# Optimization experiments

Hardware: AMD Instinct MI355X
Metric: run time of the kernel (lower is better)

## Reference

```python
import jax, jax.numpy as jnp
import numpy as np

EMBED = 1024
HEADS = 16
HEAD_DIM = EMBED // HEADS
BATCH = 4
SEQ = 2048


def setup_inputs() -> dict:
    key = jax.random.key(0)
    ks = jax.random.split(key, 9)
    s = 1.0 / np.sqrt(EMBED)
    inp = {
        "x": jax.random.normal(ks[0], (BATCH, SEQ, EMBED), dtype=jnp.float32),
        "Wq": jax.random.normal(ks[1], (EMBED, EMBED), dtype=jnp.float32) * s,
        "bq": jnp.zeros((EMBED,), jnp.float32),
        "Wk": jax.random.normal(ks[2], (EMBED, EMBED), dtype=jnp.float32) * s,
        "bk": jnp.zeros((EMBED,), jnp.float32),
        "Wv": jax.random.normal(ks[3], (EMBED, EMBED), dtype=jnp.float32) * s,
        "bv": jnp.zeros((EMBED,), jnp.float32),
        "Wo": jax.random.normal(ks[4], (EMBED, EMBED), dtype=jnp.float32) * s,
        "bo": jnp.zeros((EMBED,), jnp.float32),
    }
    return inp


def reference(x, Wq, bq, Wk, bk, Wv, bv, Wo, bo):
    B, S, E = x.shape
    H, D = HEADS, HEAD_DIM
    # projections (torch Linear with weight stored as [in,out] here)
    q = (x @ Wq + bq).reshape(B, S, H, D).transpose(0, 2, 1, 3)  # [B,H,S,D]
    k = (x @ Wk + bk).reshape(B, S, H, D).transpose(0, 2, 1, 3)
    v = (x @ Wv + bv).reshape(B, S, H, D).transpose(0, 2, 1, 3)
    scores = jnp.einsum('bhqd,bhkd->bhqk', q, k) * (1.0 / np.sqrt(D))
    causal = jnp.tril(jnp.ones((S, S), dtype=bool))
    scores = jnp.where(causal[None, None], scores, -jnp.inf)
    attn = jax.nn.softmax(scores, axis=-1)  # dropout p=0.0 -> identity
    out = jnp.einsum('bhqk,bhkd->bhqd', attn, v)  # [B,H,S,D]
    out = out.transpose(0, 2, 1, 3).reshape(B, S, E)
    return out @ Wo + bo
```

## Files before the change

### kernel.cpp

```cpp
#include <hip/hip_runtime.h>
#include <stdint.h>

#define EMBED 1024
#define SEQ   2048
#define BATCH 4
#define HEADS 16
#define HDIM  64
#define LDP   72

typedef unsigned short ushort_t;
typedef __bf16 bf16x8 __attribute__((ext_vector_type(8)));
typedef __bf16 bf16x4 __attribute__((ext_vector_type(4)));
typedef float  f32x4  __attribute__((ext_vector_type(4)));
typedef float  f32x16 __attribute__((ext_vector_type(16)));

#define MFMA16 __builtin_amdgcn_mfma_f32_16x16x32_bf16
#define MFMA32 __builtin_amdgcn_mfma_f32_32x32x16_bf16

typedef __attribute__((address_space(3))) uint32_t lds_u32_t;
typedef __attribute__((address_space(1))) const uint32_t glb_u32_t;

__device__ __forceinline__ void gl_lds16(const ushort_t* g, ushort_t* l) {
    __builtin_amdgcn_global_load_lds((glb_u32_t*)g, (lds_u32_t*)l, 16, 0, 0);
}

__device__ __forceinline__ ushort_t f2bf(float f) {
    union { float f; uint32_t u; } c; c.f = f;
    uint32_t u = c.u;
    return (ushort_t)((u + 0x7FFFu + ((u >> 16) & 1u)) >> 16);
}

__device__ __forceinline__ float exp2f_fast(float x) {
    float r; asm("v_exp_f32 %0, %1" : "=v"(r) : "v"(x)); return r;
}

__global__ __launch_bounds__(256)
void cast_x(const float* __restrict__ X, ushort_t* __restrict__ Xb)
{
    size_t i = ((size_t)blockIdx.x * 256 + threadIdx.x) * 8;
    ushort_t tmp[8];
    #pragma unroll
    for (int e = 0; e < 8; ++e) tmp[e] = f2bf(X[i + e]);
    *(uint4*)(Xb + i) = *(const uint4*)tmp;
}

__global__ __launch_bounds__(256)
void cast_transpose_w(const float* __restrict__ W, ushort_t* __restrict__ Wt)
{
    __shared__ ushort_t Ts[64 * 80];
    const int t = threadIdx.x;
    const int k0 = blockIdx.x * 64, n0 = blockIdx.y * 64;
    const int r = t >> 2, cs = (t & 3) * 16;
    const float* src = W + (size_t)(k0 + r) * EMBED + n0 + cs;
    #pragma unroll
    for (int e = 0; e < 16; ++e) Ts[(cs + e) * 80 + r] = f2bf(src[e]);
    __syncthreads();
    const int n = t >> 2, ks = (t & 3) * 16;
    ushort_t* dst = Wt + (size_t)(n0 + n) * EMBED + k0 + ks;
    *(uint4*)(dst)     = *(const uint4*)(&Ts[n * 80 + ks]);
    *(uint4*)(dst + 8) = *(const uint4*)(&Ts[n * 80 + ks + 8]);
}

__global__ __launch_bounds__(256)
void gemm_qkv(const ushort_t* __restrict__ A, const ushort_t* __restrict__ Bt,
              const float* __restrict__ bq, const float* __restrict__ bk,
              const float* __restrict__ bv, ushort_t* __restrict__ Cq, size_t tsz)
{
    __shared__ ushort_t As[128 * 32];
    __shared__ ushort_t Bs[128 * 32];
    const int t = threadIdx.x;
    const int wave = t >> 6, lane = t & 63;
    const int l15 = lane & 15, quad = lane >> 4;
    const int m0 = blockIdx.y * 128, n0 = blockIdx.x * 128;
    const int wm = (wave >> 1) * 64, wn = (wave & 1) * 64;
    f32x4 acc[4][4] = {};

    const int srow = wave * 32 + (lane >> 2), scol = (lane & 3) * 8;
    const ushort_t* Ag = A  + (size_t)(m0 + srow) * EMBED + scol;
    const ushort_t* Bg = Bt + (size_t)(n0 + srow) * EMBED + scol;
    ushort_t* AsW = As + wave * 1024;
    ushort_t* BsW = Bs + wave * 1024;

    for (int k0 = 0; k0 < EMBED; k0 += 32) {
        gl_lds16(Ag + k0,              AsW);
        gl_lds16(Ag + k0 + 16 * EMBED, AsW + 512);
        gl_lds16(Bg + k0,              BsW);
        gl_lds16(Bg + k0 + 16 * EMBED, BsW + 512);
        __syncthreads();

        bf16x8 af[4], bfr[4];
        #pragma unroll
        for (int mt = 0; mt < 4; ++mt)
            af[mt] = *(const bf16x8*)(&As[(wm + mt * 16 + l15) * 32 + quad * 8]);
        #pragma unroll
        for (int nt = 0; nt < 4; ++nt)
            bfr[nt] = *(const bf16x8*)(&Bs[(wn + nt * 16 + l15) * 32 + quad * 8]);
        #pragma unroll
        for (int mt = 0; mt < 4; ++mt)
            #pragma unroll
            for (int nt = 0; nt < 4; ++nt)
                acc[mt][nt] = MFMA16(af[mt], bfr[nt], acc[mt][nt], 0, 0, 0);
        __syncthreads();
    }

    const int mat = blockIdx.x >> 3;
    const float* bias = (mat == 0) ? bq : (mat == 1) ? bk : bv;
    const float scale = (mat == 0) ? 0.18033688011112042f : 1.0f;
    ushort_t* C = Cq + (size_t)mat * tsz;
    const int nc0 = (blockIdx.x & 7) * 128;
    #pragma unroll
    for (int nt = 0; nt < 4; ++nt) {
        int col = nc0 + wn + nt * 16 + l15;
        float bb = bias[col];
        #pragma unroll
        for (int mt = 0; mt < 4; ++mt)
            #pragma unroll
            for (int r = 0; r < 4; ++r) {
                int row = m0 + wm + mt * 16 + quad * 4 + r;
                C[(size_t)row * EMBED + col] = f2bf((acc[mt][nt][r] + bb) * scale);
            }
    }
}

__global__ __launch_bounds__(256)
void gemm_o(const ushort_t* __restrict__ A, const ushort_t* __restrict__ Bt,
            const float* __restrict__ bias, float* __restrict__ C)
{
    __shared__ ushort_t As[128 * 32];
    __shared__ ushort_t Bs[128 * 32];
    const int t = threadIdx.x;
    const int wave = t >> 6, lane = t & 63;
    const int l15 = lane & 15, quad = lane >> 4;
    const int m0 = blockIdx.y * 128, n0 = blockIdx.x * 128;
    const int wm = (wave >> 1) * 64, wn = (wave & 1) * 64;
    f32x4 acc[4][4] = {};

    const int srow = wave * 32 + (lane >> 2), scol = (lane & 3) * 8;
    const ushort_t* Ag = A  + (size_t)(m0 + srow) * EMBED + scol;
    const ushort_t* Bg = Bt + (size_t)(n0 + srow) * EMBED + scol;
    ushort_t* AsW = As + wave * 1024;
    ushort_t* BsW = Bs + wave * 1024;

    for (int k0 = 0; k0 < EMBED; k0 += 32) {
        gl_lds16(Ag + k0,              AsW);
        gl_lds16(Ag + k0 + 16 * EMBED, AsW + 512);
        gl_lds16(Bg + k0,              BsW);
        gl_lds16(Bg + k0 + 16 * EMBED, BsW + 512);
        __syncthreads();

        bf16x8 af[4], bfr[4];
        #pragma unroll
        for (int mt = 0; mt < 4; ++mt)
            af[mt] = *(const bf16x8*)(&As[(wm + mt * 16 + l15) * 32 + quad * 8]);
        #pragma unroll
        for (int nt = 0; nt < 4; ++nt)
            bfr[nt] = *(const bf16x8*)(&Bs[(wn + nt * 16 + l15) * 32 + quad * 8]);
        #pragma unroll
        for (int mt = 0; mt < 4; ++mt)
            #pragma unroll
            for (int nt = 0; nt < 4; ++nt)
                acc[mt][nt] = MFMA16(af[mt], bfr[nt], acc[mt][nt], 0, 0, 0);
        __syncthreads();
    }

    #pragma unroll
    for (int nt = 0; nt < 4; ++nt) {
        int col = n0 + wn + nt * 16 + l15;
        float bb = bias[col];
        #pragma unroll
        for (int mt = 0; mt < 4; ++mt)
            #pragma unroll
            for (int r = 0; r < 4; ++r) {
                int row = m0 + wm + mt * 16 + quad * 4 + r;
                C[(size_t)row * EMBED + col] = acc[mt][nt][r] + bb;
            }
    }
}

__global__ __launch_bounds__(256)
void transpose_v(const ushort_t* __restrict__ V, ushort_t* __restrict__ Vt)
{
    int blk = blockIdx.x;
    int st = blk & 31, bh = blk >> 5;
    int h = bh & 15, b = bh >> 4;
    int s0 = st * 64;
    __shared__ ushort_t Ts[64 * LDP];
    int tid = threadIdx.x;
    int r = tid >> 2, g = (tid & 3) * 8;

    const ushort_t* src = V + ((size_t)(b * SEQ + s0 + r)) * EMBED + h * HDIM;
    uint4 v0 = *(const uint4*)(src + g);
    uint4 v1 = *(const uint4*)(src + g + 32);
    const ushort_t* e0 = (const ushort_t*)&v0;
    const ushort_t* e1 = (const ushort_t*)&v1;
    #pragma unroll
    for (int e = 0; e < 8; ++e) Ts[(g + e) * LDP + r] = e0[e];
    #pragma unroll
    for (int e = 0; e < 8; ++e) Ts[(g + 32 + e) * LDP + r] = e1[e];
    __syncthreads();

    int d = tid >> 2;
    ushort_t* dst = Vt + ((size_t)bh * HDIM + d) * SEQ + s0;
    *(uint4*)(dst + g)      = *(const uint4*)(&Ts[d * LDP + g]);
    *(uint4*)(dst + g + 32) = *(const uint4*)(&Ts[d * LDP + g + 32]);
}

__global__ __launch_bounds__(512, 4)
void flash_attn(const ushort_t* __restrict__ Q, const ushort_t* __restrict__ K,
                const ushort_t* __restrict__ Vt, ushort_t* __restrict__ O)
{
    const int xcd = blockIdx.x & 7, c = blockIdx.x >> 3;
    const int p  = 15 - (c >> 3);
    const int bh = xcd * 8 + (c & 7);
    const int h = bh & 15, b = bh >> 4;
    const int t = threadIdx.x, w = t >> 6, lane = t & 63;
    const int wl = w & 3, hf = w >> 2;
    const int l31 = lane & 31, hi = lane >> 5;
    const int s = 4 * p + wl;
    const int sdiag = s >> 1;
    const int odd = s & 1;
    const int R = p + 1;
    const int jt0 = hf ? (p + 1) : 0;
    const size_t qkbase = (size_t)b * SEQ * EMBED + (size_t)h * HDIM;
    const size_t vtbase = (size_t)bh * HDIM * SEQ;

    __shared__ __attribute__((aligned(16))) ushort_t smem[32768];

    bf16x8 qb[4];
    {
        const ushort_t* qrow = Q + qkbase + (size_t)(s * 32 + l31) * EMBED + hi * 8;
        #pragma unroll
        for (int ks = 0; ks < 4; ++ks) qb[ks] = *(const bf16x8*)(qrow + ks * 16);
    }

    union { uint32_t u[4]; bf16x8 v; } onesu;
    onesu.u[0] = onesu.u[1] = onesu.u[2] = onesu.u[3] = 0x3F803F80u;
    const bf16x8 ones = onesu.v;

    const int rr = lane >> 3, cc = lane & 7;
    const ushort_t* Kg = K  + qkbase + (size_t)(jt0 * 64 + wl * 16 + rr) * EMBED + ((cc ^ rr) * 8);
    const ushort_t* Vg = Vt + vtbase + (size_t)(wl * 16 + rr) * SEQ + jt0 * 64 + ((cc ^ rr) * 8);

    f32x16 o0 = {}, o1 = {}, lac = {};
    const int swz = l31 & 7;

    {
        ushort_t* kd = smem + (hf * 2 + 0) * 4096 + wl * 1024;
        ushort_t* vd = smem + 16384 + (hf * 2 + 0) * 4096 + wl * 1024;
        gl_lds16(Kg,             kd);
        gl_lds16(Kg + 8 * EMBED, kd + 512);
        gl_lds16(Vg,             vd);
        gl_lds16(Vg + 8 * SEQ,   vd + 512);
    }

    for (int r = 0; r < R; ++r) {
        const int cur = r & 1;
        __syncthreads();

        if (r + 1 < R) {
            const ushort_t* kg = Kg + (size_t)(r + 1) * 64 * EMBED;
            const ushort_t* vg = Vg + (r + 1) * 64;
            ushort_t* kd = smem + (hf * 2 + (cur ^ 1)) * 4096 + wl * 1024;
            ushort_t* vd = smem + 16384 + (hf * 2 + (cur ^ 1)) * 4096 + wl * 1024;
            gl_lds16(kg,             kd);
            gl_lds16(kg + 8 * EMBED, kd + 512);
            gl_lds16(vg,             vd);
            gl_lds16(vg + 8 * SEQ,   vd + 512);
        }

        const int jt = jt0 + r;
        if (jt <= sdiag) {
            const ushort_t* Kst = smem + (hf * 2 + cur) * 4096;
            const ushort_t* Vst = smem + 16384 + (hf * 2 + cur) * 4096;
            const bool dg = (jt == sdiag);
            const bool skip1 = dg && !odd;

            f32x16 st0 = {}, st1 = {};
            #pragma unroll
            for (int ks = 0; ks < 4; ++ks) {
                bf16x8 k0 = *(const bf16x8*)(Kst + l31 * 64 + (((ks * 2 + hi) ^ swz) * 8));
                st0 = MFMA32(k0, qb[ks], st0, 0, 0, 0);
            }
            if (!skip1) {
                #pragma unroll
                for (int ks = 0; ks < 4; ++ks) {
                    bf16x8 k1 = *(const bf16x8*)(Kst + (32 + l31) * 64 + (((ks * 2 + hi) ^ swz) * 8));
                    st1 = MFMA32(k1, qb[ks], st1, 0, 0, 0);
                }
            }

            bf16x8 pa0 = {}, pa1 = {}, pa2 = {}, pa3 = {};
            {
                float p0[16];
                #pragma unroll
                for (int r2 = 0; r2 < 16; ++r2) p0[r2] = exp2f_fast(st0[r2]);
                if (dg && !odd) {
                    #pragma unroll
                    for (int r2 = 0; r2 < 16; ++r2) {
                        int key = (r2 & 3) + 8 * (r2 >> 2) + 4 * hi;
                        if (key > l31) p0[r2] = 0.f;
                    }
                }
                #pragma unroll
                for (int e = 0; e < 8; ++e) { pa0[e] = (__bf16)p0[e]; pa1[e] = (__bf16)p0[8 + e]; }
                if (!skip1) {
                    float p1[16];
                    #pragma unroll
                    for (int r2 = 0; r2 < 16; ++r2) p1[r2] = exp2f_fast(st1[r2]);
                    if (dg && odd) {
                        #pragma unroll
                        for (int r2 = 0; r2 < 16; ++r2) {
                            int key = (r2 & 3) + 8 * (r2 >> 2) + 4 * hi;
                            if (key > l31) p1[r2] = 0.f;
                        }
                    }
                    #pragma unroll
                    for (int e = 0; e < 8; ++e) { pa2[e] = (__bf16)p1[e]; pa3[e] = (__bf16)p1[8 + e]; }
                }
            }

            #pragma unroll
            for (int ksl = 0; ksl < 4; ++ksl) {
                if (!(ksl >= 2 && skip1)) {
                    bf16x8 pf = (ksl == 0) ? pa0 : (ksl == 1) ? pa1 : (ksl == 2) ? pa2 : pa3;
                    const int c0 = (((ksl * 2)     ^ swz) * 8) + hi * 4;
                    const int c1 = (((ksl * 2 + 1) ^ swz) * 8) + hi * 4;
                    union { bf16x4 hh[2]; bf16x8 v; } u0, u1;
                    u0.hh[0] = *(const bf16x4*)(Vst + l31 * 64 + c0);
                    u0.hh[1] = *(const bf16x4*)(Vst + l31 * 64 + c1);
                    u1.hh[0] = *(const bf16x4*)(Vst + (32 + l31) * 64 + c0);
                    u1.hh[1] = *(const bf16x4*)(Vst + (32 + l31) * 64 + c1);
                    o0  = MFMA32(pf, u0.v, o0, 0, 0, 0);
                    o1  = MFMA32(pf, u1.v, o1, 0, 0, 0);
                    lac = MFMA32(pf, ones, lac, 0, 0, 0);
                }
            }
        }
    }

    __syncthreads();
    float* Cs = (float*)smem;
    if (hf) {
        float* dst = Cs + (wl * 64 + lane) * 49;
        #pragma unroll
        for (int r2 = 0; r2 < 16; ++r2) {
            dst[r2]      = o0[r2];
            dst[16 + r2] = o1[r2];
            dst[32 + r2] = lac[r2];
        }
    }
    __syncthreads();
    if (!hf) {
        const float* src = Cs + (wl * 64 + lane) * 49;
        #pragma unroll
        for (int r2 = 0; r2 < 16; ++r2) {
            float t0 = o0[r2]  + src[r2];
            float t1 = o1[r2]  + src[16 + r2];
            float lt = lac[r2] + src[32 + r2];
            float inv = 1.0f / lt;
            int q = (r2 & 3) + 8 * (r2 >> 2) + 4 * hi;
            size_t ob = qkbase + (size_t)(s * 32 + q) * EMBED;
            O[ob + l31]      = f2bf(t0 * inv);
            O[ob + 32 + l31] = f2bf(t1 * inv);
        }
    }
}

extern "C" void kernel_launch(void* const* d_in, const int* in_sizes, int n_in,
                              void* d_out, int out_size, void* d_ws, size_t ws_size,
                              hipStream_t stream)
{
    (void)in_sizes; (void)n_in; (void)out_size; (void)ws_size;
    const float* x  = (const float*)d_in[0];
    const float* Wq = (const float*)d_in[1];
    const float* bq = (const float*)d_in[2];
    const float* Wk = (const float*)d_in[3];
    const float* bk = (const float*)d_in[4];
    const float* Wv = (const float*)d_in[5];
    const float* bv = (const float*)d_in[6];
    const float* Wo = (const float*)d_in[7];
    const float* bo = (const float*)d_in[8];
    float* out = (float*)d_out;

    const int M = BATCH * SEQ;
    size_t tsz = (size_t)M * EMBED;
    size_t wsz = (size_t)EMBED * EMBED;
    ushort_t* xb  = (ushort_t*)d_ws;
    ushort_t* Qb  = xb + tsz;
    ushort_t* Kb  = Qb + tsz;
    ushort_t* Vb  = Kb + tsz;
    ushort_t* Vt  = Vb + tsz;
    ushort_t* Wt0 = Vt + tsz;
    ushort_t* Wt1 = Wt0 + wsz;
    ushort_t* Wt2 = Wt1 + wsz;
    ushort_t* Wt3 = Wt2 + wsz;
    ushort_t* Ob  = xb;

    dim3 wg(16, 16);
    cast_x<<<4096, 256, 0, stream>>>(x, xb);
    cast_transpose_w<<<wg, 256, 0, stream>>>(Wq, Wt0);
    cast_transpose_w<<<wg, 256, 0, stream>>>(Wk, Wt1);
    cast_transpose_w<<<wg, 256, 0, stream>>>(Wv, Wt2);
    cast_transpose_w<<<wg, 256, 0, stream>>>(Wo, Wt3);

    gemm_qkv<<<dim3(24, 64), 256, 0, stream>>>(xb, Wt0, bq, bk, bv, Qb, tsz);

    transpose_v<<<BATCH * HEADS * (SEQ / 64), 256, 0, stream>>>(Vb, Vt);
    flash_attn<<<1024, 512, 0, stream>>>(Qb, Kb, Vt, Ob);

    gemm_o<<<dim3(8, 64), 256, 0, stream>>>(Ob, Wt3, bo, out);
}
```

Before: 271.2 us.

## Rewrite QKV GEMM as 256x256 double-buffered swizzled pipeline; merge weight casts

The QKV projection GEMM moves from a 128x128 tile with a single LDS buffer and full barriers to a 256x256 tile over 8 waves. It uses 64-wide K steps, XOR-swizzled LDS layout, double buffering with interleaved async global-to-LDS loads, and s_setprio around the MFMA clusters. Blocks are remapped so neighbouring blocks on different XCDs share tiles. The four weight cast-transpose launches are merged into one 3D-grid launch. The aim is to hide memory latency and cut launch overhead, at the cost of high LDS use (128KB per block) and register pressure.

```diff
diff --git a/kernel.cpp b/kernel.cpp
--- a/kernel.cpp
+++ b/kernel.cpp
@@ -45,8 +45,13 @@
 }
 
 __global__ __launch_bounds__(256)
-void cast_transpose_w(const float* __restrict__ W, ushort_t* __restrict__ Wt)
-{
+void cast_transpose_w4(const float* __restrict__ W0, const float* __restrict__ W1,
+                       const float* __restrict__ W2, const float* __restrict__ W3,
+                       ushort_t* __restrict__ WtAll)
+{
+    const int z = blockIdx.z;
+    const float* W = (z == 0) ? W0 : (z == 1) ? W1 : (z == 2) ? W2 : W3;
+    ushort_t* Wt = WtAll + (size_t)z * EMBED * EMBED;
     __shared__ ushort_t Ts[64 * 80];
     const int t = threadIdx.x;
     const int k0 = blockIdx.x * 64, n0 = blockIdx.y * 64;
@@ -61,63 +66,142 @@
     *(uint4*)(dst + 8) = *(const uint4*)(&Ts[n * 80 + ks + 8]);
 }
 
-__global__ __launch_bounds__(256)
+__global__ __launch_bounds__(512, 2)
 void gemm_qkv(const ushort_t* __restrict__ A, const ushort_t* __restrict__ Bt,
               const float* __restrict__ bq, const float* __restrict__ bk,
               const float* __restrict__ bv, ushort_t* __restrict__ Cq, size_t tsz)
 {
-    __shared__ ushort_t As[128 * 32];
-    __shared__ ushort_t Bs[128 * 32];
-    const int t = threadIdx.x;
-    const int wave = t >> 6, lane = t & 63;
+    __shared__ __attribute__((aligned(16))) ushort_t AsB[2][256 * 64];
+    __shared__ __attribute__((aligned(16))) ushort_t BsB[2][256 * 64];
+    const int bid = blockIdx.x;
+    const int logical = (bid & 7) * 48 + (bid >> 3);
+    const int bm = logical / 12, bn = logical % 12;
+    const int m0 = bm * 256;
+    const int t = threadIdx.x, w = t >> 6, lane = t & 63;
+    const int wm = w >> 2, wn = w & 3;
     const int l15 = lane & 15, quad = lane >> 4;
-    const int m0 = blockIdx.y * 128, n0 = blockIdx.x * 128;
-    const int wm = (wave >> 1) * 64, wn = (wave & 1) * 64;
-    f32x4 acc[4][4] = {};
-
-    const int srow = wave * 32 + (lane >> 2), scol = (lane & 3) * 8;
-    const ushort_t* Ag = A  + (size_t)(m0 + srow) * EMBED + scol;
-    const ushort_t* Bg = Bt + (size_t)(n0 + srow) * EMBED + scol;
-    ushort_t* AsW = As + wave * 1024;
-    ushort_t* BsW = Bs + wave * 1024;
-
-    for (int k0 = 0; k0 < EMBED; k0 += 32) {
-        gl_lds16(Ag + k0,              AsW);
-        gl_lds16(Ag + k0 + 16 * EMBED, AsW + 512);
-        gl_lds16(Bg + k0,              BsW);
-        gl_lds16(Bg + k0 + 16 * EMBED, BsW + 512);
-        __syncthreads();
-
-        bf16x8 af[4], bfr[4];
-        #pragma unroll
-        for (int mt = 0; mt < 4; ++mt)
-            af[mt] = *(const bf16x8*)(&As[(wm + mt * 16 + l15) * 32 + quad * 8]);
-        #pragma unroll
-        for (int nt = 0; nt < 4; ++nt)
-            bfr[nt] = *(const bf16x8*)(&Bs[(wn + nt * 16 + l15) * 32 + quad * 8]);
-        #pragma unroll
-        for (int mt = 0; mt < 4; ++mt)
-            #pragma unroll
-            for (int nt = 0; nt < 4; ++nt)
-                acc[mt][nt] = MFMA16(af[mt], bfr[nt], acc[mt][nt], 0, 0, 0);
-        __syncthreads();
-    }
-
-    const int mat = blockIdx.x >> 3;
+    const int swz8 = l15 & 7;
+
+    f32x4 acc[8][4] = {};
+
+    const int rl = lane >> 3;
+    const int srcc = ((lane & 7) ^ rl) * 8;
+    const ushort_t* Abase = A  + (size_t)(m0 + w * 8 + rl) * EMBED + srcc;
+    const ushort_t* Bbase = Bt + (size_t)(bn * 256 + w * 8 + rl) * EMBED + srcc;
+
+#define STAGE(gbase, lds, tile, half) do {                                        \
+        const ushort_t* _g = (gbase) + (size_t)(half) * 128 * EMBED + (tile) * 64; \
+        ushort_t* _d = (lds) + ((half) * 128 + w * 8) * 64;                        \
+        gl_lds16(_g, _d);                                                          \
+        gl_lds16(_g + 64 * EMBED, _d + 64 * 64);                                   \
+    } while (0)
+
+    STAGE(Bbase, BsB[0], 0, 0);
+    STAGE(Bbase, BsB[0], 0, 1);
+    STAGE(Abase, AsB[0], 0, 0);
+    STAGE(Abase, AsB[0], 0, 1);
+    STAGE(Bbase, BsB[1], 1, 0);
+    STAGE(Bbase, BsB[1], 1, 1);
+    asm volatile("s_waitcnt vmcnt(4)" ::: "memory");
+    asm volatile("s_barrier" ::: "memory");
+
+    for (int kt = 0; kt < 16; ++kt) {
+        const int cb = kt & 1, nb = cb ^ 1;
+        const ushort_t* As_ = AsB[cb];
+        const ushort_t* Bs_ = BsB[cb];
+        bf16x8 af[4][2], bLo[2][2], bHi[2][2];
+
+        #pragma unroll
+        for (int m = 0; m < 4; ++m)
+            #pragma unroll
+            for (int ks = 0; ks < 2; ++ks)
+                af[m][ks] = *(const bf16x8*)(As_ + (wm * 128 + m * 16 + l15) * 64 + (((ks * 4 + quad) ^ swz8) * 8));
+        #pragma unroll
+        for (int n = 0; n < 2; ++n)
+            #pragma unroll
+            for (int ks = 0; ks < 2; ++ks)
+                bLo[n][ks] = *(const bf16x8*)(Bs_ + (wn * 64 + n * 16 + l15) * 64 + (((ks * 4 + quad) ^ swz8) * 8));
+        if (kt + 1 < 16) STAGE(Abase, AsB[nb], kt + 1, 0);
+        asm volatile("s_barrier" ::: "memory");
+        __builtin_amdgcn_s_setprio(1);
+        #pragma unroll
+        for (int m = 0; m < 4; ++m)
+            #pragma unroll
+            for (int n = 0; n < 2; ++n) {
+                acc[m][n] = MFMA16(af[m][0], bLo[n][0], acc[m][n], 0, 0, 0);
+                acc[m][n] = MFMA16(af[m][1], bLo[n][1], acc[m][n], 0, 0, 0);
+            }
+        __builtin_amdgcn_s_setprio(0);
+        asm volatile("s_barrier" ::: "memory");
+
+        #pragma unroll
+        for (int n = 0; n < 2; ++n)
+            #pragma unroll
+            for (int ks = 0; ks < 2; ++ks)
+                bHi[n][ks] = *(const bf16x8*)(Bs_ + (wn * 64 + (n + 2) * 16 + l15) * 64 + (((ks * 4 + quad) ^ swz8) * 8));
+        if (kt + 1 < 16) STAGE(Abase, AsB[nb], kt + 1, 1);
+        asm volatile("s_barrier" ::: "memory");
+        __builtin_amdgcn_s_setprio(1);
+        #pragma unroll
+        for (int m = 0; m < 4; ++m)
+            #pragma unroll
+            for (int n = 0; n < 2; ++n) {
+                acc[m][n + 2] = MFMA16(af[m][0], bHi[n][0], acc[m][n + 2], 0, 0, 0);
+                acc[m][n + 2] = MFMA16(af[m][1], bHi[n][1], acc[m][n + 2], 0, 0, 0);
+            }
+        __builtin_amdgcn_s_setprio(0);
+        asm volatile("s_barrier" ::: "memory");
+
+        #pragma unroll
+        for (int m = 0; m < 4; ++m)
+            #pragma unroll
+            for (int ks = 0; ks < 2; ++ks)
+                af[m][ks] = *(const bf16x8*)(As_ + (wm * 128 + (m + 4) * 16 + l15) * 64 + (((ks * 4 + quad) ^ swz8) * 8));
+        if (kt + 2 < 16) STAGE(Bbase, BsB[cb], kt + 2, 0);
+        asm volatile("s_barrier" ::: "memory");
+        __builtin_amdgcn_s_setprio(1);
+        #pragma unroll
+        for (int m = 0; m < 4; ++m)
+            #pragma unroll
+            for (int n = 0; n < 2; ++n) {
+                acc[m + 4][n + 2] = MFMA16(af[m][0], bHi[n][0], acc[m + 4][n + 2], 0, 0, 0);
+                acc[m + 4][n + 2] = MFMA16(af[m][1], bHi[n][1], acc[m + 4][n + 2], 0, 0, 0);
+            }
+        __builtin_amdgcn_s_setprio(0);
+        asm volatile("s_barrier" ::: "memory");
+
+        if (kt + 2 < 16) STAGE(Bbase, BsB[cb], kt + 2, 1);
+        asm volatile("s_barrier" ::: "memory");
+        __builtin_amdgcn_s_setprio(1);
+        #pragma unroll
+        for (int m = 0; m < 4; ++m)
+            #pragma unroll
+            for (int n = 0; n < 2; ++n) {
+                acc[m + 4][n] = MFMA16(af[m][0], bLo[n][0], acc[m + 4][n], 0, 0, 0);
+                acc[m + 4][n] = MFMA16(af[m][1], bLo[n][1], acc[m + 4][n], 0, 0, 0);
+            }
+        __builtin_amdgcn_s_setprio(0);
+        if (kt == 14)      asm volatile("s_waitcnt vmcnt(0)" ::: "memory");
+        else if (kt < 14)  asm volatile("s_waitcnt vmcnt(4)" ::: "memory");
+        asm volatile("s_barrier" ::: "memory");
+    }
+#undef STAGE
+
+    const int mat = bn >> 2;
     const float* bias = (mat == 0) ? bq : (mat == 1) ? bk : bv;
     const float scale = (mat == 0) ? 0.18033688011112042f : 1.0f;
     ushort_t* C = Cq + (size_t)mat * tsz;
-    const int nc0 = (blockIdx.x & 7) * 128;
-    #pragma unroll
-    for (int nt = 0; nt < 4; ++nt) {
-        int col = nc0 + wn + nt * 16 + l15;
+    const int nc0 = (bn & 3) * 256;
+    #pragma unroll
+    for (int n = 0; n < 4; ++n) {
+        int col = nc0 + wn * 64 + n * 16 + l15;
         float bb = bias[col];
         #pragma unroll
-        for (int mt = 0; mt < 4; ++mt)
+        for (int m = 0; m < 8; ++m)
             #pragma unroll
             for (int r = 0; r < 4; ++r) {
-                int row = m0 + wm + mt * 16 + quad * 4 + r;
-                C[(size_t)row * EMBED + col] = f2bf((acc[mt][nt][r] + bb) * scale);
+                int row = m0 + wm * 128 + m * 16 + quad * 4 + r;
+                C[(size_t)row * EMBED + col] = f2bf((acc[m][n][r] + bb) * scale);
             }
     }
 }
@@ -391,19 +475,13 @@
     ushort_t* Vb  = Kb + tsz;
     ushort_t* Vt  = Vb + tsz;
     ushort_t* Wt0 = Vt + tsz;
-    ushort_t* Wt1 = Wt0 + wsz;
-    ushort_t* Wt2 = Wt1 + wsz;
-    ushort_t* Wt3 = Wt2 + wsz;
+    ushort_t* Wt3 = Wt0 + 3 * wsz;
     ushort_t* Ob  = xb;
 
-    dim3 wg(16, 16);
     cast_x<<<4096, 256, 0, stream>>>(x, xb);
-    cast_transpose_w<<<wg, 256, 0, stream>>>(Wq, Wt0);
-    cast_transpose_w<<<wg, 256, 0, stream>>>(Wk, Wt1);
-    cast_transpose_w<<<wg, 256, 0, stream>>>(Wv, Wt2);
-    cast_transpose_w<<<wg, 256, 0, stream>>>(Wo, Wt3);
-
-    gemm_qkv<<<dim3(24, 64), 256, 0, stream>>>(xb, Wt0, bq, bk, bv, Qb, tsz);
+    cast_transpose_w4<<<dim3(16, 16, 4), 256, 0, stream>>>(Wq, Wk, Wv, Wo, Wt0);
+
+    gemm_qkv<<<384, 512, 0, stream>>>(xb, Wt0, bq, bk, bv, Qb, tsz);
 
     transpose_v<<<BATCH * HEADS * (SEQ / 64), 256, 0, stream>>>(Vb, Vt);
     flash_attn<<<1024, 512, 0, stream>>>(Qb, Kb, Vt, Ob);
```

After: 275.8 us. No clear change (+1.7%).

## Fuse V transpose into QKV GEMM epilogue and batch weight casts into one launch

Applied to the files above, without the earlier changes.

The QKV GEMM's V-output blocks now stage their tile in LDS transposed and write V directly in the [b,h,d,s] layout that flash attention reads. This removes the separate transpose_v kernel and its full read and write of V. The four weight cast-transpose launches are merged into a single 3D-grid launch, removing three kernel launches. The GEMM's shared memory grows to about 34KB, which may reduce occupancy of the QKV GEMM.

```diff
diff --git a/kernel.cpp b/kernel.cpp
--- a/kernel.cpp
+++ b/kernel.cpp
@@ -6,7 +6,6 @@
 #define BATCH 4
 #define HEADS 16
 #define HDIM  64
-#define LDP   72
 
 typedef unsigned short ushort_t;
 typedef __bf16 bf16x8 __attribute__((ext_vector_type(8)));
@@ -45,8 +44,13 @@
 }
 
 __global__ __launch_bounds__(256)
-void cast_transpose_w(const float* __restrict__ W, ushort_t* __restrict__ Wt)
-{
+void cast_transpose_w4(const float* __restrict__ W0, const float* __restrict__ W1,
+                       const float* __restrict__ W2, const float* __restrict__ W3,
+                       ushort_t* __restrict__ WtAll)
+{
+    const int z = blockIdx.z;
+    const float* W = (z == 0) ? W0 : (z == 1) ? W1 : (z == 2) ? W2 : W3;
+    ushort_t* Wt = WtAll + (size_t)z * EMBED * EMBED;
     __shared__ ushort_t Ts[64 * 80];
     const int t = threadIdx.x;
     const int k0 = blockIdx.x * 64, n0 = blockIdx.y * 64;
@@ -64,7 +68,95 @@
 __global__ __launch_bounds__(256)
 void gemm_qkv(const ushort_t* __restrict__ A, const ushort_t* __restrict__ Bt,
               const float* __restrict__ bq, const float* __restrict__ bk,
-              const float* __restrict__ bv, ushort_t* __restrict__ Cq, size_t tsz)
+              const float* __restrict__ bv, ushort_t* __restrict__ Cq, size_t tsz,
+              ushort_t* __restrict__ VtOut)
+{
+    __shared__ __attribute__((aligned(16))) ushort_t arena[17408];
+    ushort_t* As = arena;
+    ushort_t* Bs = arena + 4096;
+    const int t = threadIdx.x;
+    const int wave = t >> 6, lane = t & 63;
+    const int l15 = lane & 15, quad = lane >> 4;
+    const int m0 = blockIdx.y * 128, n0 = blockIdx.x * 128;
+    const int wm = (wave >> 1) * 64, wn = (wave & 1) * 64;
+    f32x4 acc[4][4] = {};
+
+    const int srow = wave * 32 + (lane >> 2), scol = (lane & 3) * 8;
+    const ushort_t* Ag = A  + (size_t)(m0 + srow) * EMBED + scol;
+    const ushort_t* Bg = Bt + (size_t)(n0 + srow) * EMBED + scol;
+    ushort_t* AsW = As + wave * 1024;
+    ushort_t* BsW = Bs + wave * 1024;
+
+    for (int k0 = 0; k0 < EMBED; k0 += 32) {
+        gl_lds16(Ag + k0,              AsW);
+        gl_lds16(Ag + k0 + 16 * EMBED, AsW + 512);
+        gl_lds16(Bg + k0,              BsW);
+        gl_lds16(Bg + k0 + 16 * EMBED, BsW + 512);
+        __syncthreads();
+
+        bf16x8 af[4], bfr[4];
+        #pragma unroll
+        for (int mt = 0; mt < 4; ++mt)
+            af[mt] = *(const bf16x8*)(&As[(wm + mt * 16 + l15) * 32 + quad * 8]);
+        #pragma unroll
+        for (int nt = 0; nt < 4; ++nt)
+            bfr[nt] = *(const bf16x8*)(&Bs[(wn + nt * 16 + l15) * 32 + quad * 8]);
+        #pragma unroll
+        for (int mt = 0; mt < 4; ++mt)
+            #pragma unroll
+            for (int nt = 0; nt < 4; ++nt)
+                acc[mt][nt] = MFMA16(af[mt], bfr[nt], acc[mt][nt], 0, 0, 0);
+        __syncthreads();
+    }
+
+    const int mat = blockIdx.x >> 3;
+    const int nc0 = (blockIdx.x & 7) * 128;
+
+    if (mat != 2) {
+        const float* bias = (mat == 0) ? bq : bk;
+        const float scale = (mat == 0) ? 0.18033688011112042f : 1.0f;
+        ushort_t* C = Cq + (size_t)mat * tsz;
+        #pragma unroll
+        for (int nt = 0; nt < 4; ++nt) {
+            int col = nc0 + wn + nt * 16 + l15;
+            float bb = bias[col];
+            #pragma unroll
+            for (int mt = 0; mt < 4; ++mt)
+                #pragma unroll
+                for (int r = 0; r < 4; ++r) {
+                    int row = m0 + wm + mt * 16 + quad * 4 + r;
+                    C[(size_t)row * EMBED + col] = f2bf((acc[mt][nt][r] + bb) * scale);
+                }
+        }
+    } else {
+        #pragma unroll
+        for (int nt = 0; nt < 4; ++nt) {
+            int col_local = wn + nt * 16 + l15;
+            float bb = bv[nc0 + col_local];
+            #pragma unroll
+            for (int mt = 0; mt < 4; ++mt)
+                #pragma unroll
+                for (int r = 0; r < 4; ++r) {
+                    int row_local = wm + mt * 16 + quad * 4 + r;
+                    arena[col_local * 136 + row_local] = f2bf(acc[mt][nt][r] + bb);
+                }
+        }
+        __syncthreads();
+        const int hh0 = (blockIdx.x & 7) * 2;
+        const int b = m0 >> 11, s0 = m0 & 2047;
+        const int line = t >> 1, half = t & 1;
+        const int head = hh0 + (line >> 6), d = line & 63;
+        ushort_t* dst = VtOut + ((size_t)((b * 16 + head) * 64 + d)) * SEQ + s0 + half * 64;
+        const ushort_t* srcp = &arena[line * 136 + half * 64];
+        #pragma unroll
+        for (int j = 0; j < 8; ++j)
+            *(uint4*)(dst + j * 8) = *(const uint4*)(srcp + j * 8);
+    }
+}
+
+__global__ __launch_bounds__(256)
+void gemm_o(const ushort_t* __restrict__ A, const ushort_t* __restrict__ Bt,
+            const float* __restrict__ bias, float* __restrict__ C)
 {
     __shared__ ushort_t As[128 * 32];
     __shared__ ushort_t Bs[128 * 32];
@@ -103,66 +195,6 @@
         __syncthreads();
     }
 
-    const int mat = blockIdx.x >> 3;
-    const float* bias = (mat == 0) ? bq : (mat == 1) ? bk : bv;
-    const float scale = (mat == 0) ? 0.18033688011112042f : 1.0f;
-    ushort_t* C = Cq + (size_t)mat * tsz;
-    const int nc0 = (blockIdx.x & 7) * 128;
-    #pragma unroll
-    for (int nt = 0; nt < 4; ++nt) {
-        int col = nc0 + wn + nt * 16 + l15;
-        float bb = bias[col];
-        #pragma unroll
-        for (int mt = 0; mt < 4; ++mt)
-            #pragma unroll
-            for (int r = 0; r < 4; ++r) {
-                int row = m0 + wm + mt * 16 + quad * 4 + r;
-                C[(size_t)row * EMBED + col] = f2bf((acc[mt][nt][r] + bb) * scale);
-            }
-    }
-}
-
-__global__ __launch_bounds__(256)
-void gemm_o(const ushort_t* __restrict__ A, const ushort_t* __restrict__ Bt,
-            const float* __restrict__ bias, float* __restrict__ C)
-{
-    __shared__ ushort_t As[128 * 32];
-    __shared__ ushort_t Bs[128 * 32];
-    const int t = threadIdx.x;
-    const int wave = t >> 6, lane = t & 63;
-    const int l15 = lane & 15, quad = lane >> 4;
-    const int m0 = blockIdx.y * 128, n0 = blockIdx.x * 128;
-    const int wm = (wave >> 1) * 64, wn = (wave & 1) * 64;
-    f32x4 acc[4][4] = {};
-
-    const int srow = wave * 32 + (lane >> 2), scol = (lane & 3) * 8;
-    const ushort_t* Ag = A  + (size_t)(m0 + srow) * EMBED + scol;
-    const ushort_t* Bg = Bt + (size_t)(n0 + srow) * EMBED + scol;
-    ushort_t* AsW = As + wave * 1024;
-    ushort_t* BsW = Bs + wave * 1024;
-
-    for (int k0 = 0; k0 < EMBED; k0 += 32) {
-        gl_lds16(Ag + k0,              AsW);
-        gl_lds16(Ag + k0 + 16 * EMBED, AsW + 512);
-        gl_lds16(Bg + k0,              BsW);
-        gl_lds16(Bg + k0 + 16 * EMBED, BsW + 512);
-        __syncthreads();
-
-        bf16x8 af[4], bfr[4];
-        #pragma unroll
-        for (int mt = 0; mt < 4; ++mt)
-            af[mt] = *(const bf16x8*)(&As[(wm + mt * 16 + l15) * 32 + quad * 8]);
-        #pragma unroll
-        for (int nt = 0; nt < 4; ++nt)
-            bfr[nt] = *(const bf16x8*)(&Bs[(wn + nt * 16 + l15) * 32 + quad * 8]);
-        #pragma unroll
-        for (int mt = 0; mt < 4; ++mt)
-            #pragma unroll
-            for (int nt = 0; nt < 4; ++nt)
-                acc[mt][nt] = MFMA16(af[mt], bfr[nt], acc[mt][nt], 0, 0, 0);
-        __syncthreads();
-    }
-
     #pragma unroll
     for (int nt = 0; nt < 4; ++nt) {
         int col = n0 + wn + nt * 16 + l15;
@@ -175,34 +207,6 @@
                 C[(size_t)row * EMBED + col] = acc[mt][nt][r] + bb;
             }
     }
-}
-
-__global__ __launch_bounds__(256)
-void transpose_v(const ushort_t* __restrict__ V, ushort_t* __restrict__ Vt)
-{
-    int blk = blockIdx.x;
-    int st = blk & 31, bh = blk >> 5;
-    int h = bh & 15, b = bh >> 4;
-    int s0 = st * 64;
-    __shared__ ushort_t Ts[64 * LDP];
-    int tid = threadIdx.x;
-    int r = tid >> 2, g = (tid & 3) * 8;
-
-    const ushort_t* src = V + ((size_t)(b * SEQ + s0 + r)) * EMBED + h * HDIM;
-    uint4 v0 = *(const uint4*)(src + g);
-    uint4 v1 = *(const uint4*)(src + g + 32);
-    const ushort_t* e0 = (const ushort_t*)&v0;
-    const ushort_t* e1 = (const ushort_t*)&v1;
-    #pragma unroll
-    for (int e = 0; e < 8; ++e) Ts[(g + e) * LDP + r] = e0[e];
-    #pragma unroll
-    for (int e = 0; e < 8; ++e) Ts[(g + 32 + e) * LDP + r] = e1[e];
-    __syncthreads();
-
-    int d = tid >> 2;
-    ushort_t* dst = Vt + ((size_t)bh * HDIM + d) * SEQ + s0;
-    *(uint4*)(dst + g)      = *(const uint4*)(&Ts[d * LDP + g]);
-    *(uint4*)(dst + g + 32) = *(const uint4*)(&Ts[d * LDP + g + 32]);
 }
 
 __global__ __launch_bounds__(512, 4)
@@ -391,21 +395,14 @@
     ushort_t* Vb  = Kb + tsz;
     ushort_t* Vt  = Vb + tsz;
     ushort_t* Wt0 = Vt + tsz;
-    ushort_t* Wt1 = Wt0 + wsz;
-    ushort_t* Wt2 = Wt1 + wsz;
-    ushort_t* Wt3 = Wt2 + wsz;
+    ushort_t* Wt3 = Wt0 + 3 * wsz;
     ushort_t* Ob  = xb;
 
-    dim3 wg(16, 16);
     cast_x<<<4096, 256, 0, stream>>>(x, xb);
-    cast_transpose_w<<<wg, 256, 0, stream>>>(Wq, Wt0);
-    cast_transpose_w<<<wg, 256, 0, stream>>>(Wk, Wt1);
-    cast_transpose_w<<<wg, 256, 0, stream>>>(Wv, Wt2);
-    cast_transpose_w<<<wg, 256, 0, stream>>>(Wo, Wt3);
-
-    gemm_qkv<<<dim3(24, 64), 256, 0, stream>>>(xb, Wt0, bq, bk, bv, Qb, tsz);
-
-    transpose_v<<<BATCH * HEADS * (SEQ / 64), 256, 0, stream>>>(Vb, Vt);
+    cast_transpose_w4<<<dim3(16, 16, 4), 256, 0, stream>>>(Wq, Wk, Wv, Wo, Wt0);
+
+    gemm_qkv<<<dim3(24, 64), 256, 0, stream>>>(xb, Wt0, bq, bk, bv, Qb, tsz, Vt);
+
     flash_attn<<<1024, 512, 0, stream>>>(Qb, Kb, Vt, Ob);
 
     gemm_o<<<dim3(8, 64), 256, 0, stream>>>(Ob, Wt3, bo, out);
```

After: 270.4 us. Within noise of the previous version (-0.3%).
